# Optimization experiments

Hardware: AMD Instinct MI355X
Metric: run time of the kernel (lower is better)

## Reference

```python
import jax, jax.numpy as jnp
import numpy as np

EPS = 1e-5

def _conv1x1(w, x):
    # w: [out,in], x: [b,in,h,w] -> [b,out,h,w]
    return jnp.einsum('oi,bihw->bohw', w, x)

def _aggregate(resp, persp, t_w, p_w, g_w, z_w, gamma, beta):
    t = _conv1x1(t_w, persp)                      # b,c,h,w
    b, c, h, w = t.shape
    tq = t.reshape(b, c, h * w).transpose(0, 2, 1)            # b,N,c
    p = _conv1x1(p_w, resp).reshape(b, c, -1)                 # b,c,M
    g = _conv1x1(g_w, resp).reshape(b, c, -1).transpose(0, 2, 1)  # b,M,c
    att = jax.nn.softmax(jnp.einsum('bnc,bcm->bnm', tq, p), axis=2)  # b,N,M
    out = jnp.einsum('bnm,bmc->bnc', att, g)                  # b,N,c
    # faithful to torch: .contiguous().view(b,c,h,w) with NO permute
    out = out.reshape(b, c, h, w)
    z = _conv1x1(z_w, out)                                    # b,Cp,h,w
    mean = z.mean(axis=(0, 2, 3), keepdims=True)
    var = z.var(axis=(0, 2, 3), keepdims=True)                # biased (train-mode BN)
    zn = (z - mean) / jnp.sqrt(var + EPS)
    return zn * gamma[None, :, None, None] + beta[None, :, None, None]

def setup_inputs() -> dict:
    key = jax.random.key(0)
    ks = jax.random.split(key, 32)
    Cp, Cr, planes = 256, [64, 256, 512, 1024, 2048], 64
    hw = [48, 48, 24, 12, 6]
    d = {}
    d['perspective'] = jax.random.normal(ks[0], (4, Cp, 48, 48), jnp.float32)
    for i in range(5):
        d[f'response{i}'] = jax.random.normal(ks[1 + i], (4, Cr[i], hw[i], hw[i]), jnp.float32)
    d['t_w'] = jax.random.normal(ks[6], (planes, Cp), jnp.float32) * 0.05
    d['z_w'] = jax.random.normal(ks[7], (Cp, planes), jnp.float32) * 0.05
    for i in range(5):
        d[f'p{i}_w'] = jax.random.normal(ks[8 + 2 * i], (planes, Cr[i]), jnp.float32) * 0.05
        d[f'g{i}_w'] = jax.random.normal(ks[9 + 2 * i], (planes, Cr[i]), jnp.float32) * 0.05
        d[f'bn{i}_g'] = jnp.ones((Cp,), jnp.float32)
        d[f'bn{i}_b'] = jnp.zeros((Cp,), jnp.float32)
    return d

def reference(perspective, response0, response1, response2, response3, response4,
              t_w, z_w,
              p0_w, g0_w, bn0_g, bn0_b,
              p1_w, g1_w, bn1_g, bn1_b,
              p2_w, g2_w, bn2_g, bn2_b,
              p3_w, g3_w, bn3_g, bn3_b,
              p4_w, g4_w, bn4_g, bn4_b):
    resps = [response0, response1, response2, response3, response4]
    ps = [p0_w, p1_w, p2_w, p3_w, p4_w]
    gs = [g0_w, g1_w, g2_w, g3_w, g4_w]
    gms = [bn0_g, bn1_g, bn2_g, bn3_g, bn4_g]
    bts = [bn0_b, bn1_b, bn2_b, bn3_b, bn4_b]
    out = None
    for i in range(5):
        o = _aggregate(resps[i], perspective, t_w, ps[i], gs[i], z_w, gms[i], bts[i])
        out = o if out is None else out + o
    return out
```

## Files before the change

### kernel.cpp

```cpp
#include <hip/hip_runtime.h>
#include <hip/hip_bf16.h>
#include <string.h>

#define BB 4
#define CPc 256
#define NN 2304

typedef __attribute__((ext_vector_type(8))) short bf16x8;
typedef __attribute__((ext_vector_type(4))) float f32x4;

__device__ __forceinline__ short f2b(float x) {
    __hip_bfloat16 h = __float2bfloat16(x);
    return *reinterpret_cast<short*>(&h);
}
__device__ __forceinline__ float b2f16(short v) {
    union { float f; unsigned u; } x;
    x.u = ((unsigned)(unsigned short)v) << 16;
    return x.f;
}

__global__ __launch_bounds__(256) void k_wcvt(
    const float* __restrict__ t_w, const float* __restrict__ z_w,
    const float* p0, const float* p1, const float* p2, const float* p3, const float* p4,
    const float* g0, const float* g1, const float* g2, const float* g3, const float* g4,
    short* __restrict__ TWb, short* __restrict__ ZWb,
    short* __restrict__ WPb, short* __restrict__ WGb) {
    int idx = blockIdx.x * 256 + threadIdx.x;
    if (idx < 16384) { TWb[idx] = f2b(t_w[idx]); return; }
    if (idx < 32768) { ZWb[idx - 16384] = f2b(z_w[idx - 16384]); return; }
    int k = idx - 32768;
    bool isP = k < 249856;
    if (!isP) k -= 249856;
    int i, off;
    if (k < 4096)        { i = 0; off = 0; }
    else if (k < 20480)  { i = 1; off = 4096; }
    else if (k < 53248)  { i = 2; off = 20480; }
    else if (k < 118784) { i = 3; off = 53248; }
    else                 { i = 4; off = 118784; }
    const float* s;
    if (isP) s = (i == 0) ? p0 : (i == 1) ? p1 : (i == 2) ? p2 : (i == 3) ? p3 : p4;
    else     s = (i == 0) ? g0 : (i == 1) ? g1 : (i == 2) ? g2 : (i == 3) ? g3 : g4;
    (isP ? WPb : WGb)[k] = f2b(s[k - off]);
}

__global__ __launch_bounds__(256) void k_conv(
    const float* __restrict__ persp,
    const float* r0, const float* r1, const float* r2, const float* r3, const float* r4,
    const short* __restrict__ TWb, const short* __restrict__ WPb, const short* __restrict__ WGb,
    short* __restrict__ TQb, short* __restrict__ PTb, short* __restrict__ GTb,
    float* __restrict__ PPART, float* __restrict__ GPART) {
    const int CUM[7]  = {0, 144, 288, 432, 504, 552, 584};
    const int CRs[6]  = {256, 64, 256, 512, 1024, 2048};
    const int Mus[6]  = {2304, 2304, 2304, 576, 144, 36};
    const int Mps[6]  = {2304, 2304, 2304, 576, 192, 64};
    const int KSs[6]  = {1, 1, 1, 2, 4, 8};
    const int WOFF[6] = {0, 0, 4096, 20480, 53248, 118784};
    const int POFF[6] = {0, 0, 589824, 1179648, 1327104, 1376256};
    const int PBASE[6] = {0, 0, 0, 0, 294912, 491520};

    __shared__ __align__(16) short s_a[64][72];

    int blk = blockIdx.x, t = threadIdx.x;
    int w = t >> 6, lane = t & 63, lo = lane & 15, quad = lane >> 4;
    int seg = 0;
#pragma unroll
    for (int s_ = 1; s_ <= 5; ++s_) if (blk >= CUM[s_]) seg = s_;
    int Cr = CRs[seg], M = Mus[seg], Mp = Mps[seg], KS = KSs[seg];
    const float* in = (seg == 0) ? persp : (seg == 1) ? r0 : (seg == 2) ? r1 :
                      (seg == 3) ? r2 : (seg == 4) ? r3 : r4;
    const short* wp = (seg == 0) ? TWb : WPb + WOFF[seg];
    const short* wg = WGb + WOFF[seg];
    bool has_g = (seg != 0);
    int local = blk - CUM[seg];
    int mt = Mp >> 6;
    int b = local / (mt * KS);
    int rem = local % (mt * KS);
    int m0 = (rem / KS) * 64;
    int ksi = rem % KS;
    int kLen = Cr / KS, k0 = ksi * kLen;

    int ml = t & 63;
    int ssw = (ml >> 3) & 7;
    bool mvalid = (m0 + ml) < M;
    const float* inB = in + ((size_t)b * Cr) * M + m0 + ml;

    int mrow = w * 16 + lo;
    int rsw = (mrow >> 3) & 7;

    f32x4 accP[4], accG[4];
#pragma unroll
    for (int ct = 0; ct < 4; ++ct) {
        accP[ct] = f32x4{0.f, 0.f, 0.f, 0.f};
        accG[ct] = f32x4{0.f, 0.f, 0.f, 0.f};
    }

    for (int kc = k0; kc < k0 + kLen; kc += 64) {
        __syncthreads();
#pragma unroll
        for (int r = 0; r < 8; ++r) {
            int kp = (t >> 6) + r * 4;
            int q = kp >> 2, l = kp & 3;
            float v0 = 0.f, v1 = 0.f;
            if (mvalid) {
                v0 = inB[(size_t)(kc + 2 * kp) * M];
                v1 = inB[(size_t)(kc + 2 * kp + 1) * M];
            }
            short2 pk; pk.x = f2b(v0); pk.y = f2b(v1);
            *(short2*)&s_a[ml][(q ^ ssw) * 8 + l * 2] = pk;
        }
        __syncthreads();
        const bf16x8 fr0 = *(const bf16x8*)&s_a[mrow][8 * (quad ^ rsw)];
        const bf16x8 fr1 = *(const bf16x8*)&s_a[mrow][8 * ((4 + quad) ^ rsw)];
#pragma unroll
        for (int ct = 0; ct < 4; ++ct) {
            const bf16x8 fp0 = *(const bf16x8*)&wp[(size_t)(ct * 16 + lo) * Cr + kc + quad * 8];
            const bf16x8 fp1 = *(const bf16x8*)&wp[(size_t)(ct * 16 + lo) * Cr + kc + 32 + quad * 8];
            accP[ct] = __builtin_amdgcn_mfma_f32_16x16x32_bf16(fr0, fp0, accP[ct], 0, 0, 0);
            accP[ct] = __builtin_amdgcn_mfma_f32_16x16x32_bf16(fr1, fp1, accP[ct], 0, 0, 0);
            if (has_g) {
                const bf16x8 fg0 = *(const bf16x8*)&wg[(size_t)(ct * 16 + lo) * Cr + kc + quad * 8];
                const bf16x8 fg1 = *(const bf16x8*)&wg[(size_t)(ct * 16 + lo) * Cr + kc + 32 + quad * 8];
                accG[ct] = __builtin_amdgcn_mfma_f32_16x16x32_bf16(fg0, fr0, accG[ct], 0, 0, 0);
                accG[ct] = __builtin_amdgcn_mfma_f32_16x16x32_bf16(fg1, fr1, accG[ct], 0, 0, 0);
            }
        }
    }
    if (KS == 1) {
        short* outP = (seg == 0) ? TQb : PTb + POFF[seg];
        short* outG = GTb + POFF[seg];
        int mP = m0 + w * 16 + quad * 4;
#pragma unroll
        for (int ct = 0; ct < 4; ++ct) {
            int c = ct * 16 + lo;
#pragma unroll
            for (int rg = 0; rg < 4; ++rg)
                outP[((size_t)b * Mp + mP + rg) * 64 + c] = f2b(accP[ct][rg]);
        }
        if (has_g) {
            int mG = m0 + w * 16 + lo;
#pragma unroll
            for (int ct = 0; ct < 4; ++ct) {
                int cG = ct * 16 + quad * 4;
#pragma unroll
                for (int rg = 0; rg < 4; ++rg)
                    outG[((size_t)b * 64 + cG + rg) * Mp + mG] = f2b(accG[ct][rg]);
            }
        }
    } else {
        int NP = 4 * Mp * 64;
        float* pp = PPART + PBASE[seg] + (size_t)ksi * NP;
        float* gp = GPART + PBASE[seg] + (size_t)ksi * NP;
        int mP = m0 + w * 16 + quad * 4;
#pragma unroll
        for (int ct = 0; ct < 4; ++ct) {
            int c = ct * 16 + lo;
#pragma unroll
            for (int rg = 0; rg < 4; ++rg)
                pp[((size_t)b * Mp + mP + rg) * 64 + c] = accP[ct][rg];
        }
        int mG = m0 + w * 16 + lo;
#pragma unroll
        for (int ct = 0; ct < 4; ++ct) {
            int cG = ct * 16 + quad * 4;
#pragma unroll
            for (int rg = 0; rg < 4; ++rg)
                gp[((size_t)b * 64 + cG + rg) * Mp + mG] = accG[ct][rg];
        }
    }
}

__global__ __launch_bounds__(256) void k_cvt(const float* __restrict__ PPART,
                                             const float* __restrict__ GPART,
                                             short* __restrict__ PTb, short* __restrict__ GTb) {
    const int EC[4]    = {0, 147456, 196608, 212992};
    const int KSv[3]   = {2, 4, 8};
    const int PBASEv[3] = {0, 294912, 491520};
    const int POFFv[3] = {1179648, 1327104, 1376256};
    int e = blockIdx.x * 256 + threadIdx.x;
    int sg = (e < EC[1]) ? 0 : (e < EC[2]) ? 1 : 2;
    int rem = e - EC[sg];
    int KS = KSv[sg];
    int NP = (sg == 0) ? 147456 : (sg == 1) ? 49152 : 16384;
    {
        const float* src = PPART + PBASEv[sg] + rem;
        float p = 0.f;
        for (int s = 0; s < KS; ++s) p += src[(size_t)s * NP];
        PTb[POFFv[sg] + rem] = f2b(p);
    }
    {
        const float* src = GPART + PBASEv[sg] + rem;
        float g = 0.f;
        for (int s = 0; s < KS; ++s) g += src[(size_t)s * NP];
        GTb[POFFv[sg] + rem] = f2b(g);
    }
}

__global__ __launch_bounds__(256) void k_attn(const short* __restrict__ tq,
                                              const short* __restrict__ PTb,
                                              const short* __restrict__ GTb,
                                              short* __restrict__ OUTb,
                                              float* __restrict__ PNUM,
                                              float* __restrict__ PL) {
    const int AM[5]    = {2304, 2304, 576, 144, 36};
    const int AMp[5]   = {2304, 2304, 576, 192, 64};
    const int APOFF[5] = {0, 589824, 1179648, 1327104, 1376256};

    __shared__ __align__(16) short s_P[4][32][72];

    int t = threadIdx.x;
    int bid = blockIdx.x;
    int seg, r, p;
    if (bid < 576) { seg = bid / 288; int wi = bid % 288; p = wi / 72; r = wi % 72; }
    else           { int q = bid - 576; seg = 2 + q / 72; r = q % 72; p = 0; }
    int b = r / 18;
    int n0 = (r % 18) * 128;
    int M = AM[seg], Mp = AMp[seg];
    const short* pT = PTb + APOFF[seg];
    const short* gT = GTb + APOFF[seg];

    int w = t >> 6, lane = t & 63, lo = lane & 15, quad = lane >> 4;
    bool domask = (M != Mp);
    bool split = (seg < 2);
    int n0w = n0 + w * 32;

    int c0, c1;
    if (split) { c0 = p * 9; c1 = c0 + 9; }
    else       { c0 = 0; c1 = Mp >> 6; }

    const short* tqB = tq + ((size_t)b * NN + n0w + lo) * 64 + quad * 8;
    bf16x8 bq[2][2];
#pragma unroll
    for (int i = 0; i < 2; ++i)
#pragma unroll
        for (int h = 0; h < 2; ++h)
            bq[i][h] = *(const bf16x8*)(tqB + i * 16 * 64 + h * 32);

    const short* pBase = pT + ((size_t)b * Mp + lo) * 64 + quad * 8;
    const short* gBase = gT + ((size_t)b * 64 + lo) * Mp + quad * 8;

    f32x4 accO[2][4];
#pragma unroll
    for (int i = 0; i < 2; ++i)
#pragma unroll
        for (int cs = 0; cs < 4; ++cs)
            accO[i][cs] = f32x4{0.f, 0.f, 0.f, 0.f};
    float lsum[2] = {0.f, 0.f};

    short (*sp)[72] = s_P[w];

    for (int ch = c0; ch < c1; ++ch) {
        int m0 = ch << 6;
        bf16x8 pa[4][2];
#pragma unroll
        for (int ms = 0; ms < 4; ++ms)
#pragma unroll
            for (int h = 0; h < 2; ++h)
                pa[ms][h] = *(const bf16x8*)(pBase + (size_t)(m0 + ms * 16) * 64 + h * 32);
        bf16x8 gb[4][2];
#pragma unroll
        for (int cs = 0; cs < 4; ++cs)
#pragma unroll
            for (int h = 0; h < 2; ++h)
                gb[cs][h] = *(const bf16x8*)(gBase + (size_t)(cs * 16) * Mp + m0 + h * 32);

        f32x4 S[2][4];
#pragma unroll
        for (int i = 0; i < 2; ++i)
#pragma unroll
            for (int ms = 0; ms < 4; ++ms) {
                S[i][ms] = f32x4{0.f, 0.f, 0.f, 0.f};
                S[i][ms] = __builtin_amdgcn_mfma_f32_16x16x32_bf16(pa[ms][0], bq[i][0], S[i][ms], 0, 0, 0);
                S[i][ms] = __builtin_amdgcn_mfma_f32_16x16x32_bf16(pa[ms][1], bq[i][1], S[i][ms], 0, 0, 0);
            }
        if (domask) {
#pragma unroll
            for (int ms = 0; ms < 4; ++ms)
#pragma unroll
                for (int rg = 0; rg < 4; ++rg) {
                    bool oob = (m0 + ms * 16 + quad * 4 + rg) >= M;
                    if (oob) { S[0][ms][rg] = -1e30f; S[1][ms][rg] = -1e30f; }
                }
        }
#pragma unroll
        for (int i = 0; i < 2; ++i)
#pragma unroll
            for (int ms = 0; ms < 4; ++ms) {
                short4 pw;
#pragma unroll
                for (int rg = 0; rg < 4; ++rg) {
                    float e = __expf(S[i][ms][rg] - 40.f);
                    lsum[i] += e;
                    ((short*)&pw)[rg] = f2b(e);
                }
                *(short4*)&sp[i * 16 + lo][ms * 16 + quad * 4] = pw;
            }
        bf16x8 pf[2][2];
#pragma unroll
        for (int i = 0; i < 2; ++i)
#pragma unroll
            for (int h = 0; h < 2; ++h)
                pf[i][h] = *(const bf16x8*)&sp[i * 16 + lo][h * 32 + quad * 8];
#pragma unroll
        for (int i = 0; i < 2; ++i)
#pragma unroll
            for (int cs = 0; cs < 4; ++cs) {
                accO[i][cs] = __builtin_amdgcn_mfma_f32_16x16x32_bf16(pf[i][0], gb[cs][0], accO[i][cs], 0, 0, 0);
                accO[i][cs] = __builtin_amdgcn_mfma_f32_16x16x32_bf16(pf[i][1], gb[cs][1], accO[i][cs], 0, 0, 0);
            }
    }
#pragma unroll
    for (int i = 0; i < 2; ++i) {
        lsum[i] += __shfl_xor(lsum[i], 16, 64);
        lsum[i] += __shfl_xor(lsum[i], 32, 64);
    }
    if (split) {
        float* np = PNUM + ((size_t)((seg * 4 + p) * 72 + r)) * 8192;
        float* lp = PL + ((size_t)((seg * 4 + p) * 72 + r)) * 128;
        if (quad == 0) {
            lp[w * 32 + lo] = lsum[0];
            lp[w * 32 + 16 + lo] = lsum[1];
        }
#pragma unroll
        for (int i = 0; i < 2; ++i)
#pragma unroll
            for (int cs = 0; cs < 4; ++cs)
#pragma unroll
                for (int rg = 0; rg < 4; ++rg) {
                    int nl = w * 32 + i * 16 + quad * 4 + rg;
                    np[nl * 64 + cs * 16 + lo] = accO[i][cs][rg];
                }
    } else {
        short* outm = OUTb + (size_t)seg * 589824;
#pragma unroll
        for (int i = 0; i < 2; ++i)
#pragma unroll
            for (int rg = 0; rg < 4; ++rg) {
                float lt = __shfl(lsum[i], quad * 4 + rg, 64);
                int n = n0w + i * 16 + quad * 4 + rg;
#pragma unroll
                for (int cs = 0; cs < 4; ++cs)
                    outm[((size_t)b * NN + n) * 64 + cs * 16 + lo] = f2b(accO[i][cs][rg] / lt);
            }
    }
}

__global__ __launch_bounds__(256) void k_comb(const float* __restrict__ PNUM,
                                              const float* __restrict__ PL,
                                              short* __restrict__ OUTb) {
    int e4 = (blockIdx.x * 256 + threadIdx.x) * 4;
    int s = e4 / 589824;
    int rem = e4 % 589824;
    int row = rem / 64;
    int c = rem % 64;
    int b = row / 2304;
    int ng = row % 2304;
    int nblk = ng >> 7;
    int nl = ng & 127;
    int r = b * 18 + nblk;
    float ax = 0.f, ay = 0.f, az = 0.f, aw = 0.f, l = 0.f;
#pragma unroll
    for (int pp = 0; pp < 4; ++pp) {
        size_t base = (size_t)((s * 4 + pp) * 72 + r);
        const float4 v = *(const float4*)&PNUM[base * 8192 + nl * 64 + c];
        ax += v.x; ay += v.y; az += v.z; aw += v.w;
        l += PL[base * 128 + nl];
    }
    short4 o;
    o.x = f2b(ax / l);
    o.y = f2b(ay / l);
    o.z = f2b(az / l);
    o.w = f2b(aw / l);
    *(short4*)&OUTb[e4] = o;
}

__global__ __launch_bounds__(256) void k_z(const short* __restrict__ OUTb,
                                           const short* __restrict__ ZWb,
                                           short* __restrict__ Zb,
                                           float* __restrict__ PART) {
    __shared__ __align__(16) short s_ut[64][72];
    int t = threadIdx.x;
    int seg = blockIdx.x / 144;
    int r = blockIdx.x % 144;
    int b = r / 36;
    int sp0 = (r % 36) * 64;
    const short* F = OUTb + (size_t)seg * 589824 + (size_t)b * 147456;
    short* z = Zb + (size_t)seg * 2359296 + (size_t)b * 589824;
    float* part = PART + (size_t)(seg * 144 + r) * 512;

    int w = t >> 6, lane = t & 63, lo = lane & 15, quad = lane >> 4;

    bf16x8 af[4][2];
#pragma unroll
    for (int qt = 0; qt < 4; ++qt)
#pragma unroll
        for (int h = 0; h < 2; ++h)
            af[qt][h] = *(const bf16x8*)&ZWb[(size_t)(w * 64 + qt * 16 + lo) * 64 + h * 32 + quad * 8];

#pragma unroll
    for (int rr = 0; rr < 4; ++rr) {
        int idx = t + rr * 256;
        int spl = idx & 63;
        int cp0 = (idx >> 6) << 2;
        short4 pk;
        pk.x = F[(size_t)(cp0 + 0) * 2304 + sp0 + spl];
        pk.y = F[(size_t)(cp0 + 1) * 2304 + sp0 + spl];
        pk.z = F[(size_t)(cp0 + 2) * 2304 + sp0 + spl];
        pk.w = F[(size_t)(cp0 + 3) * 2304 + sp0 + spl];
        *(short4*)&s_ut[spl][cp0] = pk;
    }
    __syncthreads();

    bf16x8 bfr[4][2];
#pragma unroll
    for (int st = 0; st < 4; ++st)
#pragma unroll
        for (int h = 0; h < 2; ++h)
            bfr[st][h] = *(const bf16x8*)&s_ut[st * 16 + lo][h * 32 + quad * 8];

    f32x4 acc[4][4];
#pragma unroll
    for (int qt = 0; qt < 4; ++qt)
#pragma unroll
        for (int st = 0; st < 4; ++st) {
            acc[qt][st] = f32x4{0.f, 0.f, 0.f, 0.f};
            acc[qt][st] = __builtin_amdgcn_mfma_f32_16x16x32_bf16(af[qt][0], bfr[st][0], acc[qt][st], 0, 0, 0);
            acc[qt][st] = __builtin_amdgcn_mfma_f32_16x16x32_bf16(af[qt][1], bfr[st][1], acc[qt][st], 0, 0, 0);
        }

#pragma unroll
    for (int qt = 0; qt < 4; ++qt) {
        float s1[4] = {0.f, 0.f, 0.f, 0.f};
        float s2[4] = {0.f, 0.f, 0.f, 0.f};
        int qb = w * 64 + qt * 16 + quad * 4;
#pragma unroll
        for (int st = 0; st < 4; ++st) {
            int sp = sp0 + st * 16 + lo;
#pragma unroll
            for (int rg = 0; rg < 4; ++rg) {
                float v = acc[qt][st][rg];
                z[(size_t)(qb + rg) * 2304 + sp] = f2b(v);
                s1[rg] += v;
                s2[rg] += v * v;
            }
        }
#pragma unroll
        for (int rg = 0; rg < 4; ++rg) {
            for (int o = 8; o >= 1; o >>= 1) {
                s1[rg] += __shfl_xor(s1[rg], o, 16);
                s2[rg] += __shfl_xor(s2[rg], o, 16);
            }
            if (lo == 0) {
                float2 v2; v2.x = s1[rg]; v2.y = s2[rg];
                *(float2*)&part[(size_t)(qb + rg) * 2] = v2;
            }
        }
    }
}

__global__ __launch_bounds__(256) void k_stats(const float* __restrict__ PART,
                                               float* __restrict__ STATS) {
    int seg = blockIdx.x;
    int q = threadIdx.x;
    const float* p = PART + (size_t)seg * 144 * 512 + q * 2;
    float s1 = 0.f, s2 = 0.f;
#pragma unroll 16
    for (int blk = 0; blk < 144; ++blk) {
        float2 v = *(const float2*)&p[(size_t)blk * 512];
        s1 += v.x; s2 += v.y;
    }
    STATS[seg * 512 + q * 2] = s1;
    STATS[seg * 512 + q * 2 + 1] = s2;
}

__global__ __launch_bounds__(256) void k_final(
    const short* __restrict__ Zb, const float* __restrict__ STATS,
    const float* g0, const float* g1, const float* g2, const float* g3, const float* g4,
    const float* b0, const float* b1, const float* b2, const float* b3, const float* b4,
    float* __restrict__ outp) {
    int idx4 = (blockIdx.x * 256 + threadIdx.x) * 4;
    int q = (idx4 / NN) & 255;
    const float inv = 1.f / (float)(BB * NN);
    float4 o = {0.f, 0.f, 0.f, 0.f};
#pragma unroll
    for (int i = 0; i < 5; ++i) {
        float mean = STATS[i * 512 + q * 2] * inv;
        float var = STATS[i * 512 + q * 2 + 1] * inv - mean * mean;
        float rr = rsqrtf(var + 1e-5f);
        const float* gm = (i == 0) ? g0 : (i == 1) ? g1 : (i == 2) ? g2 : (i == 3) ? g3 : g4;
        const float* bt = (i == 0) ? b0 : (i == 1) ? b1 : (i == 2) ? b2 : (i == 3) ? b3 : b4;
        float sc = rr * gm[q];
        float ofs = bt[q] - mean * sc;
        short4 zv = *(const short4*)&Zb[(size_t)i * 2359296 + idx4];
        o.x += b2f16(zv.x) * sc + ofs;
        o.y += b2f16(zv.y) * sc + ofs;
        o.z += b2f16(zv.z) * sc + ofs;
        o.w += b2f16(zv.w) * sc + ofs;
    }
    *(float4*)&outp[idx4] = o;
}

extern "C" void kernel_launch(void* const* d_in, const int* in_sizes, int n_in,
                              void* d_out, int out_size, void* d_ws, size_t ws_size,
                              hipStream_t stream) {
    const float* persp = (const float*)d_in[0];
    const float* resp[5];
    for (int i = 0; i < 5; ++i) resp[i] = (const float*)d_in[1 + i];
    const float* t_w = (const float*)d_in[6];
    const float* z_w = (const float*)d_in[7];
    const float *p_w[5], *g_w[5], *bng[5], *bnb[5];
    for (int i = 0; i < 5; ++i) {
        p_w[i] = (const float*)d_in[8 + 4 * i];
        g_w[i] = (const float*)d_in[9 + 4 * i];
        bng[i] = (const float*)d_in[10 + 4 * i];
        bnb[i] = (const float*)d_in[11 + 4 * i];
    }
    short* TQb = (short*)d_ws;
    short* TWb = TQb + 589824;
    short* ZWb = TWb + 16384;
    short* WPb = ZWb + 16384;
    short* WGb = WPb + 249856;
    short* PTb = WGb + 249856;
    short* GTb = PTb + 1392640;
    short* Zb  = GTb + 1392640;
    short* OUTb  = (short*)((float*)d_ws + 7852032);
    float* STATS = (float*)d_ws + 7852032 + 2949120;
    float* PPART = STATS + 2560;
    float* GPART = PPART + 622592;
    float* PNUM = (float*)Zb;
    float* PL   = PNUM + 4718592;

    k_wcvt<<<2080, 256, 0, stream>>>(t_w, z_w,
        p_w[0], p_w[1], p_w[2], p_w[3], p_w[4],
        g_w[0], g_w[1], g_w[2], g_w[3], g_w[4],
        TWb, ZWb, WPb, WGb);
    k_conv<<<584, 256, 0, stream>>>(persp,
        resp[0], resp[1], resp[2], resp[3], resp[4],
        TWb, WPb, WGb, TQb, PTb, GTb, PPART, GPART);
    k_cvt<<<832, 256, 0, stream>>>(PPART, GPART, PTb, GTb);
    k_attn<<<792, 256, 0, stream>>>(TQb, PTb, GTb, OUTb, PNUM, PL);
    k_comb<<<1152, 256, 0, stream>>>(PNUM, PL, OUTb);
    k_z<<<720, 256, 0, stream>>>(OUTb, ZWb, Zb, PPART);
    k_stats<<<5, 256, 0, stream>>>(PPART, STATS);
    k_final<<<2304, 256, 0, stream>>>(Zb, STATS,
        bng[0], bng[1], bng[2], bng[3], bng[4],
        bnb[0], bnb[1], bnb[2], bnb[3], bnb[4],
        (float*)d_out);
}
```

Before: 243.8 us.

## Stage P and G tiles into LDS via async global_load_lds with double buffering

The attention kernel used to have each wave load its P and G tiles straight from global memory into registers, so all four waves fetched the same tile redundantly. Now the block cooperatively stages each 64-column P/G chunk into a double-buffered, XOR-swizzled LDS tile with global_load_lds, prefetching the next chunk while the current one is computed. Sharing the tile across waves cuts global traffic, and the prefetch overlaps loads with MFMA work. In exchange it adds about 32KB of LDS (which may lower occupancy) and a block-wide barrier every iteration.

New measurement: 224.0 us. 1.09x faster.

```diff
diff --git a/kernel.cpp b/kernel.cpp
--- a/kernel.cpp
+++ b/kernel.cpp
@@ -17,6 +17,12 @@
     union { float f; unsigned u; } x;
     x.u = ((unsigned)(unsigned short)v) << 16;
     return x.f;
+}
+
+__device__ __forceinline__ void gl2lds16(const void* g, void* l) {
+    __builtin_amdgcn_global_load_lds(
+        (const __attribute__((address_space(1))) void*)g,
+        (__attribute__((address_space(3))) void*)l, 16, 0, 0);
 }
 
 __global__ __launch_bounds__(256) void k_wcvt(
@@ -205,6 +211,7 @@
     const int AMp[5]   = {2304, 2304, 576, 192, 64};
     const int APOFF[5] = {0, 589824, 1179648, 1327104, 1376256};
 
+    __shared__ __align__(16) short s_tile[2][8192];
     __shared__ __align__(16) short s_P[4][32][72];
 
     int t = threadIdx.x;
@@ -235,8 +242,8 @@
         for (int h = 0; h < 2; ++h)
             bq[i][h] = *(const bf16x8*)(tqB + i * 16 * 64 + h * 32);
 
-    const short* pBase = pT + ((size_t)b * Mp + lo) * 64 + quad * 8;
-    const short* gBase = gT + ((size_t)b * 64 + lo) * Mp + quad * 8;
+    const short* ptSeg = pT + (size_t)b * Mp * 64;
+    const short* gtSeg = gT + (size_t)b * 64 * Mp;
 
     f32x4 accO[2][4];
 #pragma unroll
@@ -248,20 +255,48 @@
 
     short (*sp)[72] = s_P[w];
 
+#define STAGE(BUF, M0)                                                          \
+    {                                                                           \
+        _Pragma("unroll")                                                       \
+        for (int j = 0; j < 2; ++j) {                                           \
+            int slab = w * 2 + j;                                               \
+            int Bb = slab * 1024 + lane * 16;                                   \
+            int srcb = Bb ^ (((Bb >> 7) & 7) << 4);                             \
+            gl2lds16((const char*)(ptSeg + (size_t)(M0) * 64) + srcb,           \
+                     &s_tile[BUF][slab * 512]);                                 \
+        }                                                                       \
+        _Pragma("unroll")                                                       \
+        for (int j = 0; j < 2; ++j) {                                           \
+            int slab = w * 2 + j;                                               \
+            int row = slab * 8 + (lane >> 3);                                   \
+            int colb = (lane & 7) * 16;                                         \
+            int colbs = colb ^ ((row & 7) << 4);                                \
+            gl2lds16((const char*)(gtSeg + (size_t)row * Mp + (M0)) + colbs,    \
+                     &s_tile[BUF][4096 + slab * 512]);                          \
+        }                                                                       \
+    }
+
+    int buf = 0;
+    STAGE(0, c0 << 6);
+    __syncthreads();
+
+    int swz = (lo & 7) << 4;
     for (int ch = c0; ch < c1; ++ch) {
         int m0 = ch << 6;
-        bf16x8 pa[4][2];
+        bool more = (ch + 1 < c1);
+        if (more) STAGE(buf ^ 1, m0 + 64);
+
+        const char* ptL = (const char*)&s_tile[buf][0];
+        const char* gtL = (const char*)&s_tile[buf][4096];
+        bf16x8 pa[4][2], gb[4][2];
 #pragma unroll
         for (int ms = 0; ms < 4; ++ms)
 #pragma unroll
-            for (int h = 0; h < 2; ++h)
-                pa[ms][h] = *(const bf16x8*)(pBase + (size_t)(m0 + ms * 16) * 64 + h * 32);
-        bf16x8 gb[4][2];
-#pragma unroll
-        for (int cs = 0; cs < 4; ++cs)
-#pragma unroll
-            for (int h = 0; h < 2; ++h)
-                gb[cs][h] = *(const bf16x8*)(gBase + (size_t)(cs * 16) * Mp + m0 + h * 32);
+            for (int h = 0; h < 2; ++h) {
+                int A = (ms * 16 + lo) * 128 + h * 64 + quad * 16;
+                pa[ms][h] = *(const bf16x8*)(ptL + (A ^ swz));
+                gb[ms][h] = *(const bf16x8*)(gtL + (A ^ swz));
+            }
 
         f32x4 S[2][4];
 #pragma unroll
@@ -307,7 +342,10 @@
                 accO[i][cs] = __builtin_amdgcn_mfma_f32_16x16x32_bf16(pf[i][0], gb[cs][0], accO[i][cs], 0, 0, 0);
                 accO[i][cs] = __builtin_amdgcn_mfma_f32_16x16x32_bf16(pf[i][1], gb[cs][1], accO[i][cs], 0, 0, 0);
             }
-    }
+        __syncthreads();
+        buf ^= 1;
+    }
+#undef STAGE
 #pragma unroll
     for (int i = 0; i < 2; ++i) {
         lsum[i] += __shfl_xor(lsum[i], 16, 64);
```
